# Kernel optimization log

Hardware: AMD Instinct MI355X
Metric: run time of the kernel (lower is better)

Reference implementation:

```python
import jax, jax.numpy as jnp
import numpy as np

OUT_H, OUT_W = 384, 384


def _affine_grid(theta, out_h, out_w):
    # theta: [B, 2, 3]. Normalized target grid in [-1, 1], homogeneous coords.
    ys = jnp.linspace(-1.0, 1.0, out_h)
    xs = jnp.linspace(-1.0, 1.0, out_w)
    gy, gx = jnp.meshgrid(ys, xs, indexing='ij')            # [out_h, out_w]
    ones = jnp.ones_like(gx)
    grid = jnp.stack([gx.ravel(), gy.ravel(), ones.ravel()])  # [3, out_h*out_w]
    src = jnp.einsum('bij,jn->bin', theta, grid)              # [B, 2, N]
    return src[:, 0, :], src[:, 1, :]                         # x, y in [-1,1]


def _bilinear_sample(img, x, y):
    # img: [B, Hi, Wi, C]; x, y: [B, N] normalized coords in [-1, 1]
    B, Hi, Wi, C = img.shape
    x = (x + 1.0) * (Wi - 1) * 0.5
    y = (y + 1.0) * (Hi - 1) * 0.5
    x0f = jnp.floor(x)
    y0f = jnp.floor(y)
    x0 = jnp.clip(x0f.astype(jnp.int32), 0, Wi - 1)
    x1 = jnp.clip(x0f.astype(jnp.int32) + 1, 0, Wi - 1)
    y0 = jnp.clip(y0f.astype(jnp.int32), 0, Hi - 1)
    y1 = jnp.clip(y0f.astype(jnp.int32) + 1, 0, Hi - 1)
    # interpolation weights from unclipped fractional parts
    wx1 = x - x0f
    wx0 = 1.0 - wx1
    wy1 = y - y0f
    wy0 = 1.0 - wy1
    flat = img.reshape(B, Hi * Wi, C)

    def gather(yy, xx):
        idx = yy * Wi + xx                                   # [B, N]
        return jnp.take_along_axis(flat, idx[:, :, None], axis=1)  # [B, N, C]

    out = (gather(y0, x0) * (wy0 * wx0)[:, :, None]
           + gather(y0, x1) * (wy0 * wx1)[:, :, None]
           + gather(y1, x0) * (wy1 * wx0)[:, :, None]
           + gather(y1, x1) * (wy1 * wx1)[:, :, None])
    return out


def reference(X, W_loc, b_loc):
    # Localization net: global average pool over HW, then linear -> theta [B, 6]
    B, Hi, Wi, C = X.shape
    feat = X.mean(axis=(1, 2))                               # [B, C]
    theta = (feat @ W_loc + b_loc).reshape(B, 2, 3)
    x, y = _affine_grid(theta, OUT_H, OUT_W)                 # [B, N] each
    out = _bilinear_sample(X, x, y)                          # [B, N, C]
    return out.reshape(B, OUT_H, OUT_W, C)


def setup_inputs() -> dict:
    key = jax.random.key(0)
    k1, k2, k3 = jax.random.split(key, 3)
    X = jax.random.normal(k1, (16, 384, 384, 32), dtype=jnp.float32)
    # small-scale locnet weights so theta stays near a mild transform
    W_loc = jax.random.normal(k2, (32, 6), dtype=jnp.float32) * 0.1
    b_loc = jnp.array([1.0, 0.0, 0.0, 0.0, 1.0, 0.0], dtype=jnp.float32) \
            + jax.random.normal(k3, (6,), dtype=jnp.float32) * 0.05
    return {"X": X, "W_loc": W_loc, "b_loc": b_loc}
```

## Files before the change

kernel.cpp:

```cpp
#include <hip/hip_runtime.h>

#define BATCH 16
#define HI 384
#define WI 384
#define CH 32
#define OUT_H 384
#define OUT_W 384
#define HW (HI * WI)
#define NBLK 64

typedef float f32x4 __attribute__((ext_vector_type(4)));

__global__ __launch_bounds__(256) void k_partial_sums(
    const float* __restrict__ X, float* __restrict__ partials) {
  const int blk = blockIdx.x;
  const int b = blk / NBLK;
  const int sub = blk % NBLK;
  const int t = threadIdx.x;
  const int c4 = t & 7;
  const int poff = t >> 3;
  const int pixels_per_blk = HW / NBLK;
  const int p0 = sub * pixels_per_blk;

  const f32x4* base = (const f32x4*)(X + (size_t)b * HW * CH);
  f32x4 acc = {0.f, 0.f, 0.f, 0.f};
#pragma unroll 4
  for (int p = p0 + poff; p < p0 + pixels_per_blk; p += 32) {
    acc += base[(size_t)p * 8 + c4];
  }

  __shared__ f32x4 sh[256];
  sh[t] = acc;
  __syncthreads();
  if (t < 8) {
    f32x4 s = {0.f, 0.f, 0.f, 0.f};
    for (int i = 0; i < 32; ++i) s += sh[i * 8 + t];
    ((f32x4*)(partials + (size_t)blk * CH))[t] = s;
  }
}

__global__ __launch_bounds__(512) void k_theta(
    const float* __restrict__ partials, const float* __restrict__ Wl,
    const float* __restrict__ bl, float* __restrict__ theta) {
  __shared__ float feat[BATCH * CH];
  const int t = threadIdx.x;
  {
    const int b = t >> 5, c = t & 31;
    float s = 0.f;
    for (int i = 0; i < NBLK; ++i)
      s += partials[((size_t)b * NBLK + i) * CH + c];
    feat[t] = s * (1.0f / (float)HW);
  }
  __syncthreads();
  if (t < BATCH * 6) {
    const int b = t / 6, j = t % 6;
    float s = bl[j];
    for (int c = 0; c < CH; ++c) s += feat[b * CH + c] * Wl[c * 6 + j];
    theta[t] = s;
  }
}

__global__ __launch_bounds__(256) void k_sample(
    const float* __restrict__ X, const float* __restrict__ theta,
    float* __restrict__ out) {
  const int q = gridDim.x >> 3;
  const int bid = blockIdx.x;
  const int blk = (bid & 7) * q + (bid >> 3);

  const int gid = blk * 256 + threadIdx.x;
  const int c4 = gid & 7;
  const int n = gid >> 3;
  const int b = n / (OUT_H * OUT_W);
  const int p = n % (OUT_H * OUT_W);
  const int oy = p / OUT_W;
  const int ox = p % OUT_W;

  const float* th = theta + b * 6;
  const float gx = fmaf((float)ox, 2.0f / (float)(OUT_W - 1), -1.0f);
  const float gy = fmaf((float)oy, 2.0f / (float)(OUT_H - 1), -1.0f);
  const float sx = th[0] * gx + th[1] * gy + th[2];
  const float sy = th[3] * gx + th[4] * gy + th[5];
  const float x = (sx + 1.0f) * 0.5f * (float)(WI - 1);
  const float y = (sy + 1.0f) * 0.5f * (float)(HI - 1);

  const float x0f = floorf(x), y0f = floorf(y);
  const float wx1 = x - x0f, wx0 = 1.0f - wx1;
  const float wy1 = y - y0f, wy0 = 1.0f - wy1;
  const int x0 = min(max((int)x0f, 0), WI - 1);
  const int x1 = min(max((int)x0f + 1, 0), WI - 1);
  const int y0 = min(max((int)y0f, 0), HI - 1);
  const int y1 = min(max((int)y0f + 1, 0), HI - 1);

  const f32x4* img = (const f32x4*)(X + (size_t)b * HW * CH);
  const f32x4 g00 = img[((size_t)y0 * WI + x0) * 8 + c4];
  const f32x4 g01 = img[((size_t)y0 * WI + x1) * 8 + c4];
  const f32x4 g10 = img[((size_t)y1 * WI + x0) * 8 + c4];
  const f32x4 g11 = img[((size_t)y1 * WI + x1) * 8 + c4];

  const float w00 = wy0 * wx0, w01 = wy0 * wx1;
  const float w10 = wy1 * wx0, w11 = wy1 * wx1;

  f32x4 r = g00 * w00 + g01 * w01 + g10 * w10 + g11 * w11;
  __builtin_nontemporal_store(r, &((f32x4*)out)[gid]);
}

extern "C" void kernel_launch(void* const* d_in, const int* in_sizes, int n_in,
                              void* d_out, int out_size, void* d_ws,
                              size_t ws_size, hipStream_t stream) {
  const float* X = (const float*)d_in[0];
  const float* Wl = (const float*)d_in[1];
  const float* bl = (const float*)d_in[2];
  float* out = (float*)d_out;

  float* partials = (float*)d_ws;
  float* theta = partials + (size_t)BATCH * NBLK * CH;

  k_partial_sums<<<BATCH * NBLK, 256, 0, stream>>>(X, partials);
  k_theta<<<1, 512, 0, stream>>>(partials, Wl, bl, theta);

  const int total = BATCH * OUT_H * OUT_W * 8;
  k_sample<<<total / 256, 256, 0, stream>>>(X, theta, out);
}
```

Measured before the change: 175.8 us.

## Fuse reduction, theta, and sampling into one cooperative persistent kernel

Replaces the three launches with one cooperative kernel of 1024 blocks. Each block computes partial channel sums, a grid sync lets block 0 compute theta, and a second grid sync starts the sampling phase. In that phase every block loops over a contiguous chunk of output pixels that share one theta. This removes two launch gaps and keeps the sampler resident, but it adds two grid-wide barriers during which only block 0 does work, and it needs all 1024 blocks to be co-resident. If the cooperative launch fails, the original three-kernel path runs instead.

```diff
diff --git a/kernel.cpp b/kernel.cpp
--- a/kernel.cpp
+++ b/kernel.cpp
@@ -1,4 +1,7 @@
 #include <hip/hip_runtime.h>
+#include <hip/hip_cooperative_groups.h>
+
+namespace cg = cooperative_groups;
 
 #define BATCH 16
 #define HI 384
@@ -7,28 +10,143 @@
 #define OUT_H 384
 #define OUT_W 384
 #define HW (HI * WI)
-#define NBLK 64
+#define GRID 1024
+#define SUBS (GRID / BATCH)
+#define NPIX (BATCH * OUT_H * OUT_W)
+#define NGID (NPIX * 8)
+#define GIDS_PER_BLK (NGID / GRID)
+#define REPS (GIDS_PER_BLK / 256)
+#define PIX_PER_CHUNK (GIDS_PER_BLK / 8)
 
 typedef float f32x4 __attribute__((ext_vector_type(4)));
+
+__device__ __forceinline__ f32x4 sample_one(const f32x4* img, int ox, int oy,
+                                            float th0, float th1, float th2,
+                                            float th3, float th4, float th5,
+                                            int c4) {
+  const float gx = fmaf((float)ox, 2.0f / (float)(OUT_W - 1), -1.0f);
+  const float gy = fmaf((float)oy, 2.0f / (float)(OUT_H - 1), -1.0f);
+  const float sx = th0 * gx + th1 * gy + th2;
+  const float sy = th3 * gx + th4 * gy + th5;
+  const float x = (sx + 1.0f) * 0.5f * (float)(WI - 1);
+  const float y = (sy + 1.0f) * 0.5f * (float)(HI - 1);
+
+  const float x0f = floorf(x), y0f = floorf(y);
+  const float wx1 = x - x0f, wx0 = 1.0f - wx1;
+  const float wy1 = y - y0f, wy0 = 1.0f - wy1;
+  const int x0 = min(max((int)x0f, 0), WI - 1);
+  const int x1 = min(max((int)x0f + 1, 0), WI - 1);
+  const int y0 = min(max((int)y0f, 0), HI - 1);
+  const int y1 = min(max((int)y0f + 1, 0), HI - 1);
+
+  const f32x4 g00 = img[((size_t)y0 * WI + x0) * 8 + c4];
+  const f32x4 g01 = img[((size_t)y0 * WI + x1) * 8 + c4];
+  const f32x4 g10 = img[((size_t)y1 * WI + x0) * 8 + c4];
+  const f32x4 g11 = img[((size_t)y1 * WI + x1) * 8 + c4];
+
+  return g00 * (wy0 * wx0) + g01 * (wy0 * wx1) + g10 * (wy1 * wx0) +
+         g11 * (wy1 * wx1);
+}
+
+__global__ __launch_bounds__(256, 4) void k_fused(
+    const float* __restrict__ X, const float* __restrict__ Wl,
+    const float* __restrict__ bl, float* __restrict__ out,
+    float* __restrict__ ws) {
+  cg::grid_group grid = cg::this_grid();
+  const int t = threadIdx.x;
+  const int blk = blockIdx.x;
+
+  float* partials = ws;
+  float* theta = ws + GRID * CH;
+
+  __shared__ f32x4 sh[256];
+  __shared__ float feat[BATCH * CH];
+
+  {
+    const int b = blk / SUBS;
+    const int sub = blk % SUBS;
+    const int c4 = t & 7;
+    const int poff = t >> 3;
+    const int ppb = HW / SUBS;
+    const int p0 = sub * ppb;
+
+    const f32x4* base = (const f32x4*)(X + (size_t)b * HW * CH);
+    f32x4 acc = {0.f, 0.f, 0.f, 0.f};
+#pragma unroll 4
+    for (int p = p0 + poff; p < p0 + ppb; p += 32) {
+      acc += base[(size_t)p * 8 + c4];
+    }
+    sh[t] = acc;
+    __syncthreads();
+    if (t < 8) {
+      f32x4 s = {0.f, 0.f, 0.f, 0.f};
+      for (int i = 0; i < 32; ++i) s += sh[i * 8 + t];
+      ((f32x4*)(partials + (size_t)blk * CH))[t] = s;
+    }
+  }
+
+  grid.sync();
+
+  if (blk == 0) {
+    for (int k = t; k < BATCH * CH; k += 256) {
+      const int b = k >> 5, c = k & 31;
+      float s = 0.f;
+      for (int i = 0; i < SUBS; ++i)
+        s += partials[((size_t)b * SUBS + i) * CH + c];
+      feat[k] = s * (1.0f / (float)HW);
+    }
+    __syncthreads();
+    if (t < BATCH * 6) {
+      const int b = t / 6, j = t % 6;
+      float s = bl[j];
+      for (int c = 0; c < CH; ++c) s += feat[b * CH + c] * Wl[c * 6 + j];
+      theta[t] = s;
+    }
+  }
+
+  grid.sync();
+
+  {
+    const int q = GRID >> 3;
+    const int chunk = (blk & 7) * q + (blk >> 3);
+    const int b = chunk / (HW / PIX_PER_CHUNK);
+
+    const float th0 = theta[b * 6 + 0], th1 = theta[b * 6 + 1],
+                th2 = theta[b * 6 + 2], th3 = theta[b * 6 + 3],
+                th4 = theta[b * 6 + 4], th5 = theta[b * 6 + 5];
+
+    const f32x4* img = (const f32x4*)(X + (size_t)b * HW * CH);
+    const int pbase = chunk * PIX_PER_CHUNK - b * (OUT_H * OUT_W);
+    const int c4 = t & 7;
+
+    for (int rep = 0; rep < REPS; ++rep) {
+      const int gid = chunk * GIDS_PER_BLK + rep * 256 + t;
+      const int lp = pbase + ((rep * 256 + t) >> 3);
+      const int oy = lp / OUT_W;
+      const int ox = lp % OUT_W;
+      f32x4 r = sample_one(img, ox, oy, th0, th1, th2, th3, th4, th5, c4);
+      __builtin_nontemporal_store(r, &((f32x4*)out)[gid]);
+    }
+  }
+}
 
 __global__ __launch_bounds__(256) void k_partial_sums(
     const float* __restrict__ X, float* __restrict__ partials) {
   const int blk = blockIdx.x;
-  const int b = blk / NBLK;
-  const int sub = blk % NBLK;
+  const int b = blk / SUBS;
+  const int sub = blk % SUBS;
   const int t = threadIdx.x;
   const int c4 = t & 7;
   const int poff = t >> 3;
-  const int pixels_per_blk = HW / NBLK;
-  const int p0 = sub * pixels_per_blk;
+  const int ppb = HW / SUBS;
+  const int p0 = sub * ppb;
 
   const f32x4* base = (const f32x4*)(X + (size_t)b * HW * CH);
   f32x4 acc = {0.f, 0.f, 0.f, 0.f};
 #pragma unroll 4
-  for (int p = p0 + poff; p < p0 + pixels_per_blk; p += 32) {
+  for (int p = p0 + poff; p < p0 + ppb; p += 32) {
     acc += base[(size_t)p * 8 + c4];
   }
-
   __shared__ f32x4 sh[256];
   sh[t] = acc;
   __syncthreads();
@@ -47,8 +165,8 @@
   {
     const int b = t >> 5, c = t & 31;
     float s = 0.f;
-    for (int i = 0; i < NBLK; ++i)
-      s += partials[((size_t)b * NBLK + i) * CH + c];
+    for (int i = 0; i < SUBS; ++i)
+      s += partials[((size_t)b * SUBS + i) * CH + c];
     feat[t] = s * (1.0f / (float)HW);
   }
   __syncthreads();
@@ -76,31 +194,9 @@
   const int ox = p % OUT_W;
 
   const float* th = theta + b * 6;
-  const float gx = fmaf((float)ox, 2.0f / (float)(OUT_W - 1), -1.0f);
-  const float gy = fmaf((float)oy, 2.0f / (float)(OUT_H - 1), -1.0f);
-  const float sx = th[0] * gx + th[1] * gy + th[2];
-  const float sy = th[3] * gx + th[4] * gy + th[5];
-  const float x = (sx + 1.0f) * 0.5f * (float)(WI - 1);
-  const float y = (sy + 1.0f) * 0.5f * (float)(HI - 1);
-
-  const float x0f = floorf(x), y0f = floorf(y);
-  const float wx1 = x - x0f, wx0 = 1.0f - wx1;
-  const float wy1 = y - y0f, wy0 = 1.0f - wy1;
-  const int x0 = min(max((int)x0f, 0), WI - 1);
-  const int x1 = min(max((int)x0f + 1, 0), WI - 1);
-  const int y0 = min(max((int)y0f, 0), HI - 1);
-  const int y1 = min(max((int)y0f + 1, 0), HI - 1);
-
   const f32x4* img = (const f32x4*)(X + (size_t)b * HW * CH);
-  const f32x4 g00 = img[((size_t)y0 * WI + x0) * 8 + c4];
-  const f32x4 g01 = img[((size_t)y0 * WI + x1) * 8 + c4];
-  const f32x4 g10 = img[((size_t)y1 * WI + x0) * 8 + c4];
-  const f32x4 g11 = img[((size_t)y1 * WI + x1) * 8 + c4];
-
-  const float w00 = wy0 * wx0, w01 = wy0 * wx1;
-  const float w10 = wy1 * wx0, w11 = wy1 * wx1;
-
-  f32x4 r = g00 * w00 + g01 * w01 + g10 * w10 + g11 * w11;
+  f32x4 r = sample_one(img, ox, oy, th[0], th[1], th[2], th[3], th[4], th[5],
+                       c4);
   __builtin_nontemporal_store(r, &((f32x4*)out)[gid]);
 }
 
@@ -111,13 +207,16 @@
   const float* Wl = (const float*)d_in[1];
   const float* bl = (const float*)d_in[2];
   float* out = (float*)d_out;
-
-  float* partials = (float*)d_ws;
-  float* theta = partials + (size_t)BATCH * NBLK * CH;
-
-  k_partial_sums<<<BATCH * NBLK, 256, 0, stream>>>(X, partials);
-  k_theta<<<1, 512, 0, stream>>>(partials, Wl, bl, theta);
-
-  const int total = BATCH * OUT_H * OUT_W * 8;
-  k_sample<<<total / 256, 256, 0, stream>>>(X, theta, out);
-}
+  float* ws = (float*)d_ws;
+
+  void* args[] = {(void*)&X, (void*)&Wl, (void*)&bl, (void*)&out, (void*)&ws};
+  hipError_t err = hipLaunchCooperativeKernel((void*)k_fused, dim3(GRID),
+                                              dim3(256), args, 0, stream);
+  if (err != hipSuccess) {
+    float* partials = ws;
+    float* theta = ws + GRID * CH;
+    k_partial_sums<<<GRID, 256, 0, stream>>>(X, partials);
+    k_theta<<<1, 512, 0, stream>>>(partials, Wl, bl, theta);
+    k_sample<<<NGID / 256, 256, 0, stream>>>(X, theta, out);
+  }
+}
```

Result: slower. 401.2 us (+128.2%).

## Tile sampler blocks as 8x4 output patches and double reduction blocks

Applied to the files above, without the earlier changes.

The sampling kernel now maps each block to an 8x4 tile of output pixels, ordered column-major over tiles with an XCD-style block swizzle, instead of a 32-pixel row strip. The aim is better 2D locality of the bilinear gathers, so that neighbouring rows share cache lines in L2. The partial-sum reduction also uses 128 blocks per image instead of 64, and the theta kernel's reduction loop is unrolled. The trade-off is that stores now cover 8-pixel row segments (1 KB contiguous) rather than fully contiguous 32-pixel runs, and there are more partials to reduce.

```diff
diff --git a/kernel.cpp b/kernel.cpp
--- a/kernel.cpp
+++ b/kernel.cpp
@@ -7,7 +7,14 @@
 #define OUT_H 384
 #define OUT_W 384
 #define HW (HI * WI)
-#define NBLK 64
+#define NBLK 128
+#define NPIX (BATCH * OUT_H * OUT_W)
+#define TILE_W 8
+#define TILE_H 4
+#define TILES_X (OUT_W / TILE_W)
+#define TILES_Y (OUT_H / TILE_H)
+#define TILES_PER_IMG (TILES_X * TILES_Y)
+#define SAMP_BLOCKS (BATCH * TILES_PER_IMG)
 
 typedef float f32x4 __attribute__((ext_vector_type(4)));
 
@@ -19,13 +26,13 @@
   const int t = threadIdx.x;
   const int c4 = t & 7;
   const int poff = t >> 3;
-  const int pixels_per_blk = HW / NBLK;
-  const int p0 = sub * pixels_per_blk;
+  const int ppb = HW / NBLK;
+  const int p0 = sub * ppb;
 
   const f32x4* base = (const f32x4*)(X + (size_t)b * HW * CH);
   f32x4 acc = {0.f, 0.f, 0.f, 0.f};
 #pragma unroll 4
-  for (int p = p0 + poff; p < p0 + pixels_per_blk; p += 32) {
+  for (int p = p0 + poff; p < p0 + ppb; p += 32) {
     acc += base[(size_t)p * 8 + c4];
   }
 
@@ -47,6 +54,7 @@
   {
     const int b = t >> 5, c = t & 31;
     float s = 0.f;
+#pragma unroll 8
     for (int i = 0; i < NBLK; ++i)
       s += partials[((size_t)b * NBLK + i) * CH + c];
     feat[t] = s * (1.0f / (float)HW);
@@ -63,17 +71,23 @@
 __global__ __launch_bounds__(256) void k_sample(
     const float* __restrict__ X, const float* __restrict__ theta,
     float* __restrict__ out) {
-  const int q = gridDim.x >> 3;
+  const int q = SAMP_BLOCKS >> 3;
   const int bid = blockIdx.x;
   const int blk = (bid & 7) * q + (bid >> 3);
 
-  const int gid = blk * 256 + threadIdx.x;
-  const int c4 = gid & 7;
-  const int n = gid >> 3;
-  const int b = n / (OUT_H * OUT_W);
-  const int p = n % (OUT_H * OUT_W);
-  const int oy = p / OUT_W;
-  const int ox = p % OUT_W;
+  const int b = blk / TILES_PER_IMG;
+  const int tl = blk % TILES_PER_IMG;
+  const int tx = tl / TILES_Y;
+  const int ty = tl % TILES_Y;
+
+  const int t = threadIdx.x;
+  const int c4 = t & 7;
+  const int px = t >> 3;
+  const int col = px & 7;
+  const int row = px >> 3;
+
+  const int ox = tx * TILE_W + col;
+  const int oy = ty * TILE_H + row;
 
   const float* th = theta + b * 6;
   const float gx = fmaf((float)ox, 2.0f / (float)(OUT_W - 1), -1.0f);
@@ -100,8 +114,10 @@
   const float w00 = wy0 * wx0, w01 = wy0 * wx1;
   const float w10 = wy1 * wx0, w11 = wy1 * wx1;
 
-  f32x4 r = g00 * w00 + g01 * w01 + g10 * w10 + g11 * w11;
-  __builtin_nontemporal_store(r, &((f32x4*)out)[gid]);
+  const f32x4 r = g00 * w00 + g01 * w01 + g10 * w10 + g11 * w11;
+
+  const size_t n = (size_t)b * (OUT_H * OUT_W) + (size_t)oy * OUT_W + ox;
+  __builtin_nontemporal_store(r, (f32x4*)out + n * 8 + c4);
 }
 
 extern "C" void kernel_launch(void* const* d_in, const int* in_sizes, int n_in,
@@ -117,7 +133,5 @@
 
   k_partial_sums<<<BATCH * NBLK, 256, 0, stream>>>(X, partials);
   k_theta<<<1, 512, 0, stream>>>(partials, Wl, bl, theta);
-
-  const int total = BATCH * OUT_H * OUT_W * 8;
-  k_sample<<<total / 256, 256, 0, stream>>>(X, theta, out);
+  k_sample<<<SAMP_BLOCKS, 256, 0, stream>>>(X, theta, out);
 }
```

Result: no change. 173.5 us (-1.3%).
